# Kernel optimization log

Hardware: AMD Instinct MI355X
Metric: run time of the kernel (lower is better)

The kernel has to match this reference:

```python
import jax, jax.numpy as jnp
import numpy as np

H = 256; S = 64; AN = 16; D = 8; HH = 8; WW = 8; T = 32; N = 64; NV = 32
HG = 2 + 3 * H  # GRU hidden = sum(parser_sections) = 1 + 1 + 3*H


def _gru(x, w_ih, w_hh, b_ih, b_hh):
    """torch-style GRU over leading axis; x: [L, N, Hin] -> [L, N, HG]."""
    def step(h, xt):
        gi = xt @ w_ih.T + b_ih
        gh = h @ w_hh.T + b_hh
        ir, iz, inn = jnp.split(gi, 3, axis=-1)
        hr, hz, hn = jnp.split(gh, 3, axis=-1)
        r = jax.nn.sigmoid(ir + hr)
        z = jax.nn.sigmoid(iz + hz)
        n = jnp.tanh(inn + r * hn)
        h2 = (1 - z) * n + z * h
        return h2, h2
    h0 = jnp.zeros((x.shape[1], w_hh.shape[1]), x.dtype)
    _, ys = jax.lax.scan(step, h0, x)
    return ys


def _cos(e, m):  # e [N,H], m [N,S,H] -> [N,S]; matches F.cosine_similarity eps=1e-8
    num = jnp.einsum('nh,nsh->ns', e, m)
    den = jnp.linalg.norm(e, axis=-1)[:, None] * jnp.linalg.norm(m, axis=-1)
    return num / jnp.maximum(den, 1e-8)


def _l1norm(x):  # F.normalize(x, p=1, dim=-1)
    return x / jnp.maximum(jnp.abs(x).sum(-1, keepdims=True), 1e-12)


def setup_inputs():
    key = jax.random.key(0)
    ks = jax.random.split(key, 16)
    sc = lambda k, shape, fan: jax.random.normal(k, shape, jnp.float32) / np.float32(np.sqrt(fan))
    return dict(
        base=jax.random.normal(ks[0], (T, N, D, HH, WW), jnp.float32),
        interactable=(jax.random.uniform(ks[1], (T, N, AN - 5)) < 0.5).astype(jnp.float32),
        rnn_hxs=jnp.zeros((1, N, 1 + AN + 1 + H + S), jnp.float32),
        emb=sc(ks[2], (NV, H), 1.0),
        gru_w_ih=sc(ks[3], (3 * HG, H), H),
        gru_w_hh=sc(ks[4], (3 * HG, HG), HG),
        gru_b_ih=jnp.zeros((3 * HG,), jnp.float32),
        gru_b_hh=jnp.zeros((3 * HG,), jnp.float32),
        conv0_w=sc(ks[5], (H, D * H), D * H),
        conv0_b=jnp.zeros((H,), jnp.float32),
        convs_w=sc(ks[6], (2, H, H), H),
        convs_b=jnp.zeros((2, H), jnp.float32),
        lin_w=sc(ks[7], (H, H * HH * WW), H * HH * WW),
        lin_b=jnp.zeros((H,), jnp.float32),
        psi_w=sc(ks[8], (H, H * AN), H * AN),
        psi_b=jnp.zeros((H,), jnp.float32),
        actor_w=sc(ks[9], (AN, H), H),
        actor_b=jnp.zeros((AN,), jnp.float32),
        critic_w=sc(ks[10], (1, H), H),
        critic_b=jnp.zeros((1,), jnp.float32),
        subtasks=jax.random.randint(ks[11], (N, S), 0, NV),
        actions=jax.random.randint(ks[12], (T, N), 0, AN),
    )


def reference(base, interactable, rnn_hxs, emb, gru_w_ih, gru_w_hh, gru_b_ih, gru_b_hh,
              conv0_w, conv0_b, convs_w, convs_b, lin_w, lin_b, psi_w, psi_b,
              actor_w, actor_b, critic_w, critic_b, subtasks, actions):
    # --- parser: GRU over the subtask token sequence ---
    rnn_in = emb[subtasks].transpose(1, 0, 2)                                    # [S, N, H]
    X = _gru(rnn_in, gru_w_ih, gru_w_hh, gru_b_ih, gru_b_hh).transpose(1, 0, 2)  # [N, S, HG]
    c, p0 = X[..., 0], X[..., 1]                                                 # [N, S]
    M = X[..., 2:2 + H]
    Mm = X[..., 2 + H:2 + 2 * H]
    Mp = X[..., 2 + 2 * H:]
    hx = rnn_hxs[0]
    new_ep = jnp.all(rnn_hxs == 0, axis=-1)[0]                                   # [N]
    p_init = jnp.where(new_ep[:, None], p0, hx[:, 1 + AN + 1 + H:])

    def f_net(base_t, r):
        n = base_t.shape[0]
        # outer product [N,H,d,h,w] -> [N, H*d, h, w], then 1x1 convs
        x = (base_t[:, None] * r[:, :, None, None, None]).reshape(n, H * D, HH, WW)
        x = jax.nn.relu(jnp.einsum('nchw,oc->nohw', x, conv0_w) + conv0_b[None, :, None, None])
        for i in range(convs_w.shape[0]):
            x = jax.nn.relu(jnp.einsum('nchw,oc->nohw', x, convs_w[i]) + convs_b[i][None, :, None, None])
        return jax.nn.relu(x.reshape(n, -1) @ lin_w.T + lin_b)

    def step(p, xs):
        base_t, inter_t, a_t = xs
        ps = jax.nn.softmax(p, axis=-1)
        r = jnp.einsum('ns,nsh->nh', ps, M)                                      # memory read
        s = f_net(base_t, r)
        dprobs = jax.nn.softmax(s @ actor_w.T + actor_b, axis=-1)
        nonzero = jnp.pad(inter_t, ((0, 0), (5, 0)), constant_values=1.0)        # [N, AN]
        probs = dprobs * nonzero
        deficit = 1.0 - probs.sum(-1, keepdims=True)
        probs = probs + _l1norm(nonzero) * deficit
        probs = _l1norm(jnp.clip(probs, 0.0, 1.0))
        a_oh = jax.nn.one_hot(a_t, AN, dtype=s.dtype)
        e = (s[:, :, None] * a_oh[:, None, :]).reshape(s.shape[0], H * AN) @ psi_w.T + psi_b
        p_new = ps + c * _cos(e, Mp) - c * _cos(e, Mm)                           # memory write
        v = s @ critic_w.T + critic_b
        out = jnp.concatenate([a_t[:, None].astype(s.dtype), probs, v, s, p_new], axis=-1)
        return p_new, out

    _, hx_out = jax.lax.scan(step, p_init, (base, interactable, actions))        # [T, N, 338]
    return hx_out, hx_out[-1:]
```

## Files before the change

kernel.cpp:

```cpp
#include <hip/hip_runtime.h>
#include <math.h>

constexpr int cH  = 256;
constexpr int cS  = 64;
constexpr int cAN = 16;
constexpr int cD  = 8;
constexpr int cT  = 32;
constexpr int cN  = 64;
constexpr int cHG = 770;
constexpr int cG3 = 2310;
constexpr int cOW = 338;
constexpr int XLD = 800;
constexpr int GLD = 832;
constexpr int MLD = 2496;
constexpr int PROW = 2560;

__global__ __launch_bounds__(256) void k_gitab(const float* __restrict__ emb,
                                               const float* __restrict__ w_ih,
                                               const float* __restrict__ b_ih,
                                               float* __restrict__ gitp) {
  int v = blockIdx.y;
  int j = blockIdx.x * 256 + threadIdx.x;
  __shared__ float es[cH];
  es[threadIdx.x] = emb[v * cH + threadIdx.x];
  __syncthreads();
  if (j < cG3) {
    float acc = b_ih[j];
    const float* wr = w_ih + (size_t)j * cH;
    #pragma unroll 8
    for (int h = 0; h < cH; ++h) acc += wr[h] * es[h];
    int g = j / cHG, kk = j - g * cHG;
    gitp[(size_t)v * MLD + g * GLD + kk] = acc;
  }
}

__global__ __launch_bounds__(256) void k_wpad(const float* __restrict__ whh,
                                              float* __restrict__ wpadG) {
  int idx = blockIdx.x * 256 + threadIdx.x;
  if (idx < PROW * XLD) {
    int row = idx / XLD, col = idx - row * XLD;
    int g = row / GLD, k = row - g * GLD;
    wpadG[idx] = (g < 3 && k < cHG && col < cHG)
                     ? whh[(size_t)(g * cHG + k) * cHG + col] : 0.f;
  }
}

__global__ __launch_bounds__(256) void k_psiperm(const float* __restrict__ psi_w,
                                                 float* __restrict__ psip) {
  int idx = blockIdx.x * 256 + threadIdx.x;
  int a = idx >> 16, h = (idx >> 8) & 255, o = idx & 255;
  psip[idx] = psi_w[((size_t)o * cH + h) * cAN + a];
}

__global__ __launch_bounds__(256) void k_gru_gemm(const float* __restrict__ wpadG,
                                                  const float* __restrict__ X,
                                                  float* __restrict__ part, int s) {
  int tid = threadIdx.x;
  int tile = blockIdx.x % 40;
  int ks   = blockIdx.x / 40;
  int g = tile / 13, kt = tile - g * 13;
  int cbase = (ks <= 2) ? ks * 13 : 38;
  int ccnt  = (ks < 2) ? 13 : 12;
  int kbase = cbase * 16;
  int csz = ccnt * 16;

  __shared__ float Bst[208][68];
  __shared__ float As[2][16][68];

  const float* bsrc = wpadG + ((size_t)(g * GLD + kt * 64)) * XLD + kbase;
  for (int i = tid; i < 64 * 208; i += 256) {
    int jl = i / 208, k2l = i - jl * 208;
    if (k2l < csz) Bst[k2l][jl] = bsrc[(size_t)jl * XLD + k2l];
  }

  int tm = tid & 15, tj = tid >> 4;
  int lrow = tid >> 2, lcol = (tid & 3) * 4;
  __syncthreads();

  float acc[4][4] = {};
  const float* Xp = X + ((size_t)lrow * cS + (s - 1)) * XLD + kbase;
  float4 av = *(const float4*)(Xp + lcol);
  for (int c = 0; c < ccnt; ++c) {
    int buf = c & 1;
    As[buf][lcol + 0][lrow] = av.x;
    As[buf][lcol + 1][lrow] = av.y;
    As[buf][lcol + 2][lrow] = av.z;
    As[buf][lcol + 3][lrow] = av.w;
    __syncthreads();
    if (c + 1 < ccnt) av = *(const float4*)(Xp + (c + 1) * 16 + lcol);
    #pragma unroll
    for (int kk = 0; kk < 16; ++kk) {
      float4 a4 = *(const float4*)&As[buf][kk][tm * 4];
      float4 b4 = *(const float4*)&Bst[c * 16 + kk][tj * 4];
      acc[0][0] += a4.x * b4.x; acc[0][1] += a4.x * b4.y; acc[0][2] += a4.x * b4.z; acc[0][3] += a4.x * b4.w;
      acc[1][0] += a4.y * b4.x; acc[1][1] += a4.y * b4.y; acc[1][2] += a4.y * b4.z; acc[1][3] += a4.y * b4.w;
      acc[2][0] += a4.z * b4.x; acc[2][1] += a4.z * b4.y; acc[2][2] += a4.z * b4.z; acc[2][3] += a4.z * b4.w;
      acc[3][0] += a4.w * b4.x; acc[3][1] += a4.w * b4.y; acc[3][2] += a4.w * b4.z; acc[3][3] += a4.w * b4.w;
    }
    __syncthreads();
  }
  float* pw = part + (size_t)ks * (64 * PROW) + (size_t)(g * GLD + kt * 64);
  #pragma unroll
  for (int i = 0; i < 4; ++i) {
    *(float4*)(pw + (size_t)(tm * 4 + i) * PROW + tj * 4) =
        make_float4(acc[i][0], acc[i][1], acc[i][2], acc[i][3]);
  }
}

__global__ __launch_bounds__(256) void k_gru_gate(const float* __restrict__ part,
                                                  const float* __restrict__ bhh,
                                                  const float* __restrict__ gitp,
                                                  const int* __restrict__ subtasks,
                                                  float* __restrict__ X, int s) {
  int kq = blockIdx.x, m = blockIdx.y, tid = threadIdx.x;
  if (tid >= 200) return;
  int k = kq * 200 + tid;
  float* xrow = X + ((size_t)m * cS + s) * XLD;
  if (k >= cHG) { if (k < XLD) xrow[k] = 0.f; return; }
  float accr = 0.f, accz = 0.f, accn = 0.f;
  if (s > 0) {
    const float* pm = part + (size_t)m * PROW;
    #pragma unroll
    for (int q = 0; q < 4; ++q) {
      const float* pq = pm + (size_t)q * (64 * PROW);
      accr += pq[k];
      accz += pq[GLD + k];
      accn += pq[2 * GLD + k];
    }
  }
  int v = subtasks[m * cS + s];
  const float* git = gitp + (size_t)v * MLD;
  float rg = 1.f / (1.f + expf(-(git[k]           + accr + bhh[k])));
  float zg = 1.f / (1.f + expf(-(git[GLD + k]     + accz + bhh[cHG + k])));
  float ng = tanhf(git[2 * GLD + k] + rg * (accn + bhh[2 * cHG + k]));
  float hp = (s > 0) ? X[((size_t)m * cS + (s - 1)) * XLD + k] : 0.f;
  xrow[k] = (1.f - zg) * ng + zg * hp;
}

__global__ __launch_bounds__(256) void k_pinit(const float* __restrict__ hxs,
                                               const float* __restrict__ X,
                                               float* __restrict__ psb,
                                               float* __restrict__ r,
                                               float* __restrict__ nMp,
                                               float* __restrict__ nMm) {
  int n = blockIdx.x, tid = threadIdx.x;
  __shared__ int anynz;
  __shared__ float pss[cS];
  __shared__ float mx, sm;
  if (tid == 0) anynz = 0;
  __syncthreads();
  int nz = (hxs[n * cOW + tid] != 0.f) ? 1 : 0;
  if (tid + 256 < cOW) nz |= (hxs[n * cOW + tid + 256] != 0.f) ? 1 : 0;
  if (nz) anynz = 1;
  __syncthreads();
  bool newep = (anynz == 0);
  if (tid < cS) {
    const float* xr = X + ((size_t)n * cS + tid) * XLD;
    float p0 = xr[1];
    float pv = newep ? p0 : hxs[n * cOW + 1 + cAN + 1 + cH + tid];
    pss[tid] = pv;
    float sp = 0.f, smn = 0.f;
    for (int h = 0; h < cH; ++h) {
      float vp = xr[2 + 2 * cH + h]; sp += vp * vp;
      float vm = xr[2 + cH + h];     smn += vm * vm;
    }
    nMp[n * cS + tid] = sqrtf(sp);
    nMm[n * cS + tid] = sqrtf(smn);
  }
  __syncthreads();
  if (tid == 0) { float m = pss[0]; for (int i = 1; i < cS; ++i) m = fmaxf(m, pss[i]); mx = m; }
  __syncthreads();
  if (tid < cS) pss[tid] = expf(pss[tid] - mx);
  __syncthreads();
  if (tid == 0) { float s = 0.f; for (int i = 0; i < cS; ++i) s += pss[i]; sm = s; }
  __syncthreads();
  if (tid < cS) { pss[tid] /= sm; psb[n * cS + tid] = pss[tid]; }
  __syncthreads();
  float acc = 0.f;
  for (int s2 = 0; s2 < cS; ++s2)
    acc += pss[s2] * X[((size_t)n * cS + s2) * XLD + 2 + tid];
  r[n * cH + tid] = acc;
}

__global__ __launch_bounds__(256) void k_front(const float* __restrict__ r,
                                               const float* __restrict__ base,
                                               const float* __restrict__ cw,
                                               const float* __restrict__ cb,
                                               float* __restrict__ x1T, int t) {
  int o = blockIdx.x, tid = threadIdx.x;
  __shared__ float rsQ[64][65][4];
  __shared__ float w0s[64][9];

  #pragma unroll
  for (int it = 0; it < 16; ++it) {
    int flat4 = it * 256 + tid;
    int n = flat4 >> 6, hq = flat4 & 63;
    float4 v = *(const float4*)(r + n * cH + hq * 4);
    *(float4*)&rsQ[hq][n][0] = v;
  }
  __syncthreads();

  {
    int dg = tid >> 6, n = tid & 63;
    int d0 = dg * 2;
    const float* cwo = cw + (size_t)o * (cD * cH);
    float acc0 = 0.f, acc1 = 0.f;
    #pragma unroll 4
    for (int hq = 0; hq < 64; ++hq) {
      float4 rv = *(const float4*)&rsQ[hq][n][0];
      #pragma unroll
      for (int j = 0; j < 4; ++j) {
        float2 w = *(const float2*)(cwo + (hq * 4 + j) * 8 + d0);
        float rvj = ((const float*)&rv)[j];
        acc0 += w.x * rvj;
        acc1 += w.y * rvj;
      }
    }
    w0s[n][d0]     = acc0;
    w0s[n][d0 + 1] = acc1;
  }
  __syncthreads();

  {
    int q = tid >> 6, n = tid & 63;
    float w0[8];
    #pragma unroll
    for (int d = 0; d < 8; ++d) w0[d] = w0s[n][d];
    float bias = cb[o];
    const float4* b4 = (const float4*)(base + ((size_t)(t * cN + n) * cD) * 64);
    float* dst = x1T + (size_t)o * 4096 + n * 64 + q * 16;
    #pragma unroll
    for (int k = 0; k < 4; ++k) {
      float4 acc = make_float4(bias, bias, bias, bias);
      #pragma unroll
      for (int d = 0; d < 8; ++d) {
        float4 bv = b4[d * 16 + q * 4 + k];
        acc.x += w0[d] * bv.x; acc.y += w0[d] * bv.y;
        acc.z += w0[d] * bv.z; acc.w += w0[d] * bv.w;
      }
      acc.x = fmaxf(acc.x, 0.f); acc.y = fmaxf(acc.y, 0.f);
      acc.z = fmaxf(acc.z, 0.f); acc.w = fmaxf(acc.w, 0.f);
      *(float4*)(dst + k * 4) = acc;
    }
  }
}

__global__ __launch_bounds__(256) void k_gemmT(const float* __restrict__ AT,
                                               const float* __restrict__ W,
                                               const float* __restrict__ bias,
                                               float* __restrict__ C, int mode) {
  int nb = blockIdx.x, mb = blockIdx.y, tid = threadIdx.x;
  int tm = tid & 15, tj = tid >> 4;
  __shared__ float As[16][68];
  __shared__ float Bs[16][68];
  float acc[4][4] = {{0.f}};
  int lrow = tid >> 2, lcol = (tid & 3) * 4;
  int kr = tid >> 4, mc4 = (tid & 15) * 4;
  for (int kc = 0; kc < cH; kc += 16) {
    float4 av = *(const float4*)(AT + (size_t)(kc + kr) * 4096 + mb * 64 + mc4);
    float4 wv = *(const float4*)(W + (size_t)(nb * 64 + lrow) * cH + kc + lcol);
    *(float4*)&As[kr][mc4] = av;
    Bs[lcol][lrow] = wv.x; Bs[lcol + 1][lrow] = wv.y; Bs[lcol + 2][lrow] = wv.z; Bs[lcol + 3][lrow] = wv.w;
    __syncthreads();
    #pragma unroll
    for (int kk = 0; kk < 16; ++kk) {
      float4 a4 = *(const float4*)&As[kk][tm * 4];
      float4 b4 = *(const float4*)&Bs[kk][tj * 4];
      acc[0][0] += a4.x * b4.x; acc[0][1] += a4.x * b4.y; acc[0][2] += a4.x * b4.z; acc[0][3] += a4.x * b4.w;
      acc[1][0] += a4.y * b4.x; acc[1][1] += a4.y * b4.y; acc[1][2] += a4.y * b4.z; acc[1][3] += a4.y * b4.w;
      acc[2][0] += a4.z * b4.x; acc[2][1] += a4.z * b4.y; acc[2][2] += a4.z * b4.z; acc[2][3] += a4.z * b4.w;
      acc[3][0] += a4.w * b4.x; acc[3][1] += a4.w * b4.y; acc[3][2] += a4.w * b4.z; acc[3][3] += a4.w * b4.w;
    }
    __syncthreads();
  }
  if (mode == 0) {
    #pragma unroll
    for (int j = 0; j < 4; ++j) {
      int o = nb * 64 + tj * 4 + j;
      float bv = bias[o];
      float4 o4;
      o4.x = fmaxf(acc[0][j] + bv, 0.f);
      o4.y = fmaxf(acc[1][j] + bv, 0.f);
      o4.z = fmaxf(acc[2][j] + bv, 0.f);
      o4.w = fmaxf(acc[3][j] + bv, 0.f);
      *(float4*)(C + (size_t)o * 4096 + mb * 64 + tm * 4) = o4;
    }
  } else {
    #pragma unroll
    for (int j = 0; j < 4; ++j) {
      int o = nb * 64 + tj * 4 + j;
      float bv = bias[o];
      float4 o4;
      o4.x = fmaxf(acc[0][j] + bv, 0.f);
      o4.y = fmaxf(acc[1][j] + bv, 0.f);
      o4.z = fmaxf(acc[2][j] + bv, 0.f);
      o4.w = fmaxf(acc[3][j] + bv, 0.f);
      *(float4*)(C + (size_t)mb * (64 * cH) + (size_t)o * 64 + tm * 4) = o4;
    }
  }
}

__global__ __launch_bounds__(256) void k_lin(const float* __restrict__ A,
                                             const float* __restrict__ W,
                                             float* __restrict__ part) {
  int nb = blockIdx.x, kcb = blockIdx.y, tid = threadIdx.x;
  int tm = tid & 15, tj = tid >> 4;
  __shared__ float As[16][68];
  __shared__ float Bs[16][68];
  float acc[4][4] = {{0.f}};
  int lrow = tid >> 2, lcol = (tid & 3) * 4;
  for (int kc = 0; kc < 256; kc += 16) {
    float4 av = *(const float4*)(A + (size_t)lrow * 16384 + kcb * 256 + kc + lcol);
    float4 wv = *(const float4*)(W + (size_t)(nb * 64 + lrow) * 16384 + kcb * 256 + kc + lcol);
    As[lcol][lrow] = av.x; As[lcol + 1][lrow] = av.y; As[lcol + 2][lrow] = av.z; As[lcol + 3][lrow] = av.w;
    Bs[lcol][lrow] = wv.x; Bs[lcol + 1][lrow] = wv.y; Bs[lcol + 2][lrow] = wv.z; Bs[lcol + 3][lrow] = wv.w;
    __syncthreads();
    #pragma unroll
    for (int kk = 0; kk < 16; ++kk) {
      float4 a4 = *(const float4*)&As[kk][tm * 4];
      float4 b4 = *(const float4*)&Bs[kk][tj * 4];
      acc[0][0] += a4.x * b4.x; acc[0][1] += a4.x * b4.y; acc[0][2] += a4.x * b4.z; acc[0][3] += a4.x * b4.w;
      acc[1][0] += a4.y * b4.x; acc[1][1] += a4.y * b4.y; acc[1][2] += a4.y * b4.z; acc[1][3] += a4.y * b4.w;
      acc[2][0] += a4.z * b4.x; acc[2][1] += a4.z * b4.y; acc[2][2] += a4.z * b4.z; acc[2][3] += a4.z * b4.w;
      acc[3][0] += a4.w * b4.x; acc[3][1] += a4.w * b4.y; acc[3][2] += a4.w * b4.z; acc[3][3] += a4.w * b4.w;
    }
    __syncthreads();
  }
  #pragma unroll
  for (int i = 0; i < 4; ++i) {
    int n = tm * 4 + i;
    float4 o4 = make_float4(acc[i][0], acc[i][1], acc[i][2], acc[i][3]);
    *(float4*)(part + ((size_t)kcb * cN + n) * cH + nb * 64 + tj * 4) = o4;
  }
}

__global__ __launch_bounds__(256) void k_tail(const float* __restrict__ part,
                                              const float* __restrict__ lin_b,
                                              const float* __restrict__ actor_w,
                                              const float* __restrict__ actor_b,
                                              const float* __restrict__ critic_w,
                                              const float* __restrict__ critic_b,
                                              const float* __restrict__ psip,
                                              const float* __restrict__ psi_b,
                                              const float* __restrict__ inter,
                                              const int* __restrict__ actions,
                                              const float* __restrict__ X,
                                              const float* __restrict__ nMp,
                                              const float* __restrict__ nMm,
                                              float* __restrict__ psb,
                                              float* __restrict__ r,
                                              float* __restrict__ out, int t) {
  int n = blockIdx.x, tid = threadIdx.x;
  __shared__ float ss[cH];
  __shared__ float es[cH];
  __shared__ float lg[cAN], dp[cAN], nzv[cAN], prb[cAN];
  __shared__ float red[256];
  __shared__ float ared[16][17];
  __shared__ float cred[2][4][64];
  __shared__ float enorm_s;
  __shared__ float pns[cS];
  __shared__ float mx2, sm2;
  float* orow = out + ((size_t)t * cN + n) * cOW;
  float acc = lin_b[tid];
  for (int kc = 0; kc < 64; ++kc) acc += part[((size_t)kc * cN + n) * cH + tid];
  float sv = fmaxf(acc, 0.f);
  ss[tid] = sv;
  orow[1 + cAN + 1 + tid] = sv;
  __syncthreads();
  {
    int a = tid & 15, hg = tid >> 4;
    float pa = 0.f;
    const float* wr = actor_w + a * cH + hg * 16;
    const float* sh = &ss[hg * 16];
    #pragma unroll
    for (int hh2 = 0; hh2 < 16; ++hh2) pa += wr[hh2] * sh[hh2];
    ared[a][hg] = pa;
  }
  __syncthreads();
  if (tid < cAN) {
    float a = actor_b[tid];
    #pragma unroll
    for (int i = 0; i < 16; ++i) a += ared[tid][i];
    lg[tid] = a;
  }
  __syncthreads();
  if (tid < cAN) {
    float m = lg[0];
    for (int i = 1; i < cAN; ++i) m = fmaxf(m, lg[i]);
    dp[tid] = expf(lg[tid] - m);
  }
  __syncthreads();
  if (tid < cAN) {
    float s = 0.f;
    for (int i = 0; i < cAN; ++i) s += dp[i];
    float dprob = dp[tid] / s;
    float nv = (tid < 5) ? 1.f : inter[((size_t)t * cN + n) * (cAN - 5) + (tid - 5)];
    nzv[tid] = nv;
    prb[tid] = dprob * nv;
  }
  __syncthreads();
  if (tid < cAN) {
    float sp = 0.f, sn = 0.f;
    for (int i = 0; i < cAN; ++i) { sp += prb[i]; sn += nzv[i]; }
    float deficit = 1.f - sp;
    float v2 = prb[tid] + (nzv[tid] / fmaxf(sn, 1e-12f)) * deficit;
    prb[tid] = fminf(fmaxf(v2, 0.f), 1.f);
  }
  __syncthreads();
  if (tid < cAN) {
    float s = 0.f;
    for (int i = 0; i < cAN; ++i) s += prb[i];
    orow[1 + tid] = prb[tid] / fmaxf(s, 1e-12f);
  }
  int at = actions[t * cN + n];
  {
    float a = psi_b[tid];
    for (int h = 0; h < cH; ++h) a += psip[((size_t)at * cH + h) * cH + tid] * ss[h];
    es[tid] = a;
    red[tid] = a * a;
  }
  __syncthreads();
  for (int st = 128; st > 0; st >>= 1) {
    if (tid < st) red[tid] += red[tid + st];
    __syncthreads();
  }
  if (tid == 0) enorm_s = sqrtf(red[0]);
  __syncthreads();
  float enorm = enorm_s;
  red[tid] = critic_w[tid] * ss[tid];
  __syncthreads();
  for (int st = 128; st > 0; st >>= 1) {
    if (tid < st) red[tid] += red[tid + st];
    __syncthreads();
  }
  if (tid == 0) {
    orow[1 + cAN] = red[0] + critic_b[0];
    orow[0] = (float)at;
  }
  {
    int s2 = tid & 63, hg = tid >> 6;
    const float* xr = X + ((size_t)n * cS + s2) * XLD;
    const float* xp = xr + 2 + 2 * cH + hg * 64;
    const float* xm = xr + 2 + cH + hg * 64;
    const float* ep = &es[hg * 64];
    float dpp = 0.f, dmm = 0.f;
    #pragma unroll 8
    for (int h2 = 0; h2 < 64; ++h2) {
      float ev = ep[h2];
      dpp += ev * xp[h2];
      dmm += ev * xm[h2];
    }
    cred[0][hg][s2] = dpp;
    cred[1][hg][s2] = dmm;
  }
  __syncthreads();
  if (tid < cS) {
    float dpp = cred[0][0][tid] + cred[0][1][tid] + cred[0][2][tid] + cred[0][3][tid];
    float dmm = cred[1][0][tid] + cred[1][1][tid] + cred[1][2][tid] + cred[1][3][tid];
    const float* xr = X + ((size_t)n * cS + tid) * XLD;
    float cP = dpp / fmaxf(enorm * nMp[n * cS + tid], 1e-8f);
    float cM = dmm / fmaxf(enorm * nMm[n * cS + tid], 1e-8f);
    float cc = xr[0];
    float pn = psb[n * cS + tid] + cc * cP - cc * cM;
    pns[tid] = pn;
    orow[1 + cAN + 1 + cH + tid] = pn;
  }
  __threadfence_block();
  __syncthreads();
  if (t == cT - 1) {
    float* orow2 = out + (size_t)cT * cN * cOW + (size_t)n * cOW;
    orow2[tid] = orow[tid];
    if (tid + 256 < cOW) orow2[tid + 256] = orow[tid + 256];
  }
  if (tid == 0) { float m2 = pns[0]; for (int i = 1; i < cS; ++i) m2 = fmaxf(m2, pns[i]); mx2 = m2; }
  __syncthreads();
  if (tid < cS) pns[tid] = expf(pns[tid] - mx2);
  __syncthreads();
  if (tid == 0) { float s2 = 0.f; for (int i = 0; i < cS; ++i) s2 += pns[i]; sm2 = s2; }
  __syncthreads();
  if (tid < cS) { pns[tid] /= sm2; psb[n * cS + tid] = pns[tid]; }
  __syncthreads();
  float acc2 = 0.f;
  for (int s2 = 0; s2 < cS; ++s2)
    acc2 += pns[s2] * X[((size_t)n * cS + s2) * XLD + 2 + tid];
  r[n * cH + tid] = acc2;
}

extern "C" void kernel_launch(void* const* d_in, const int* in_sizes, int n_in,
                              void* d_out, int out_size, void* d_ws, size_t ws_size,
                              hipStream_t stream) {
  const float* base     = (const float*)d_in[0];
  const float* inter    = (const float*)d_in[1];
  const float* hxs      = (const float*)d_in[2];
  const float* emb      = (const float*)d_in[3];
  const float* w_ih     = (const float*)d_in[4];
  const float* w_hh     = (const float*)d_in[5];
  const float* b_ih     = (const float*)d_in[6];
  const float* b_hh     = (const float*)d_in[7];
  const float* conv0_w  = (const float*)d_in[8];
  const float* conv0_b  = (const float*)d_in[9];
  const float* convs_w  = (const float*)d_in[10];
  const float* convs_b  = (const float*)d_in[11];
  const float* lin_w    = (const float*)d_in[12];
  const float* lin_b    = (const float*)d_in[13];
  const float* psi_w    = (const float*)d_in[14];
  const float* psi_b    = (const float*)d_in[15];
  const float* actor_w  = (const float*)d_in[16];
  const float* actor_b  = (const float*)d_in[17];
  const float* critic_w = (const float*)d_in[18];
  const float* critic_b = (const float*)d_in[19];
  const int*   subtasks = (const int*)d_in[20];
  const int*   actions  = (const int*)d_in[21];
  float* out = (float*)d_out;
  float* ws  = (float*)d_ws;

  float* gitp  = ws + 0;
  float* psb   = ws + 0;
  float* r     = ws + 4096;
  float* nMp   = ws + 20480;
  float* nMm   = ws + 24576;
  float* X     = ws + 79872;
  float* wpadG = ws + 3356672;
  float* psip  = ws + 3356672;
  float* x1T   = ws + 4405248;
  float* part  = x1T;
  float* partG = ws + 5404672;
  float* x2T   = ws + 5453824;
  float* x3t   = ws + 6502400;

  k_gitab<<<dim3(10, 32), 256, 0, stream>>>(emb, w_ih, b_ih, gitp);
  k_wpad<<<8000, 256, 0, stream>>>(w_hh, wpadG);
  k_gru_gate<<<dim3(4, 64), 256, 0, stream>>>(partG, b_hh, gitp, subtasks, X, 0);
  for (int s = 1; s < cS; ++s) {
    k_gru_gemm<<<160, 256, 0, stream>>>(wpadG, X, partG, s);
    k_gru_gate<<<dim3(4, 64), 256, 0, stream>>>(partG, b_hh, gitp, subtasks, X, s);
  }
  k_psiperm<<<4096, 256, 0, stream>>>(psi_w, psip);
  k_pinit<<<64, 256, 0, stream>>>(hxs, X, psb, r, nMp, nMm);
  for (int t = 0; t < cT; ++t) {
    k_front<<<256, 256, 0, stream>>>(r, base, conv0_w, conv0_b, x1T, t);
    k_gemmT<<<dim3(4, 64), 256, 0, stream>>>(x1T, convs_w, convs_b, x2T, 0);
    k_gemmT<<<dim3(4, 64), 256, 0, stream>>>(x2T, convs_w + 65536, convs_b + 256, x3t, 1);
    k_lin<<<dim3(4, 64), 256, 0, stream>>>(x3t, lin_w, part);
    k_tail<<<64, 256, 0, stream>>>(part, lin_b, actor_w, actor_b, critic_w, critic_b,
                                   psip, psi_b, inter, actions, X, nMp, nMm,
                                   psb, r, out, t);
  }
}
```

Before: 4.611 ms.

## Fuse conv0 into first conv GEMM and move r-to-weight projection into tail

Result: slower. 5.887 ms (+27.7%).

```diff
diff --git a/kernel.cpp b/kernel.cpp
--- a/kernel.cpp
+++ b/kernel.cpp
@@ -139,13 +139,16 @@
 
 __global__ __launch_bounds__(256) void k_pinit(const float* __restrict__ hxs,
                                                const float* __restrict__ X,
+                                               const float* __restrict__ cw,
                                                float* __restrict__ psb,
                                                float* __restrict__ r,
                                                float* __restrict__ nMp,
-                                               float* __restrict__ nMm) {
+                                               float* __restrict__ nMm,
+                                               float* __restrict__ w0r) {
   int n = blockIdx.x, tid = threadIdx.x;
   __shared__ int anynz;
   __shared__ float pss[cS];
+  __shared__ float rsf[cH];
   __shared__ float mx, sm;
   if (tid == 0) anynz = 0;
   __syncthreads();
@@ -180,76 +183,102 @@
   for (int s2 = 0; s2 < cS; ++s2)
     acc += pss[s2] * X[((size_t)n * cS + s2) * XLD + 2 + tid];
   r[n * cH + tid] = acc;
-}
-
-__global__ __launch_bounds__(256) void k_front(const float* __restrict__ r,
-                                               const float* __restrict__ base,
-                                               const float* __restrict__ cw,
-                                               const float* __restrict__ cb,
-                                               float* __restrict__ x1T, int t) {
-  int o = blockIdx.x, tid = threadIdx.x;
-  __shared__ float rsQ[64][65][4];
-  __shared__ float w0s[64][9];
-
+  rsf[tid] = acc;
+  __syncthreads();
+  {
+    const float* cwo = cw + (size_t)tid * (cD * cH);
+    float a0=0,a1=0,a2=0,a3=0,a4=0,a5=0,a6=0,a7=0;
+    #pragma unroll 4
+    for (int h = 0; h < cH; ++h) {
+      float rv = rsf[h];
+      float4 wa = *(const float4*)(cwo + h * 8);
+      float4 wb = *(const float4*)(cwo + h * 8 + 4);
+      a0 += wa.x * rv; a1 += wa.y * rv; a2 += wa.z * rv; a3 += wa.w * rv;
+      a4 += wb.x * rv; a5 += wb.y * rv; a6 += wb.z * rv; a7 += wb.w * rv;
+    }
+    float* wd = w0r + (size_t)n * 2048 + tid * 8;
+    *(float4*)(wd)     = make_float4(a0, a1, a2, a3);
+    *(float4*)(wd + 4) = make_float4(a4, a5, a6, a7);
+  }
+}
+
+__global__ __launch_bounds__(256) void k_conv1f(const float* __restrict__ w0r,
+                                                const float* __restrict__ base,
+                                                const float* __restrict__ cb0,
+                                                const float* __restrict__ W1,
+                                                const float* __restrict__ b1,
+                                                float* __restrict__ y1T, int t) {
+  int b = blockIdx.x, tid = threadIdx.x;
+  int n  = (b & 7) | ((b >> 5) << 3);
+  int nb = (b >> 3) & 3;
+  __shared__ float x1s[256][68];
+  __shared__ float w0s[256][9];
+  __shared__ float bs[8][64];
+  __shared__ float Bs[16][68];
+  {
+    const float* src = w0r + (size_t)n * 2048 + tid * 8;
+    float4 va = *(const float4*)(src);
+    float4 vb = *(const float4*)(src + 4);
+    *(float4*)&w0s[tid][0] = va;
+    *(float4*)&w0s[tid][4] = vb;
+    w0s[tid][8] = cb0[tid];
+  }
+  if (tid < 128) {
+    int d = tid >> 4, c4 = (tid & 15) * 4;
+    *(float4*)&bs[d][c4] =
+        *(const float4*)(base + ((size_t)(t * cN + n) * cD + d) * 64 + c4);
+  }
+  __syncthreads();
+  {
+    int wv = tid >> 6, ln = tid & 63;
+    for (int oi = 0; oi < 64; ++oi) {
+      int o = wv * 64 + oi;
+      float acc = w0s[o][8];
+      #pragma unroll
+      for (int d = 0; d < 8; ++d) acc += w0s[o][d] * bs[d][ln];
+      x1s[o][ln] = fmaxf(acc, 0.f);
+    }
+  }
+  __syncthreads();
+  int tm = tid & 15, tj = tid >> 4;
+  int lrow = tid >> 2, lcol = (tid & 3) * 4;
+  float acc[4][4] = {{0.f}};
+  for (int kc = 0; kc < cH; kc += 16) {
+    float4 wv4 = *(const float4*)(W1 + (size_t)(nb * 64 + lrow) * cH + kc + lcol);
+    Bs[lcol][lrow] = wv4.x; Bs[lcol + 1][lrow] = wv4.y;
+    Bs[lcol + 2][lrow] = wv4.z; Bs[lcol + 3][lrow] = wv4.w;
+    __syncthreads();
+    #pragma unroll
+    for (int kk = 0; kk < 16; ++kk) {
+      float4 a4 = *(const float4*)&x1s[kc + kk][tm * 4];
+      float4 b4 = *(const float4*)&Bs[kk][tj * 4];
+      acc[0][0] += a4.x * b4.x; acc[0][1] += a4.x * b4.y; acc[0][2] += a4.x * b4.z; acc[0][3] += a4.x * b4.w;
+      acc[1][0] += a4.y * b4.x; acc[1][1] += a4.y * b4.y; acc[1][2] += a4.y * b4.z; acc[1][3] += a4.y * b4.w;
+      acc[2][0] += a4.z * b4.x; acc[2][1] += a4.z * b4.y; acc[2][2] += a4.z * b4.z; acc[2][3] += a4.z * b4.w;
+      acc[3][0] += a4.w * b4.x; acc[3][1] += a4.w * b4.y; acc[3][2] += a4.w * b4.z; acc[3][3] += a4.w * b4.w;
+    }
+    __syncthreads();
+  }
   #pragma unroll
-  for (int it = 0; it < 16; ++it) {
-    int flat4 = it * 256 + tid;
-    int n = flat4 >> 6, hq = flat4 & 63;
-    float4 v = *(const float4*)(r + n * cH + hq * 4);
-    *(float4*)&rsQ[hq][n][0] = v;
-  }
-  __syncthreads();
-
-  {
-    int dg = tid >> 6, n = tid & 63;
-    int d0 = dg * 2;
-    const float* cwo = cw + (size_t)o * (cD * cH);
-    float acc0 = 0.f, acc1 = 0.f;
-    #pragma unroll 4
-    for (int hq = 0; hq < 64; ++hq) {
-      float4 rv = *(const float4*)&rsQ[hq][n][0];
-      #pragma unroll
-      for (int j = 0; j < 4; ++j) {
-        float2 w = *(const float2*)(cwo + (hq * 4 + j) * 8 + d0);
-        float rvj = ((const float*)&rv)[j];
-        acc0 += w.x * rvj;
-        acc1 += w.y * rvj;
-      }
-    }
-    w0s[n][d0]     = acc0;
-    w0s[n][d0 + 1] = acc1;
-  }
-  __syncthreads();
-
-  {
-    int q = tid >> 6, n = tid & 63;
-    float w0[8];
-    #pragma unroll
-    for (int d = 0; d < 8; ++d) w0[d] = w0s[n][d];
-    float bias = cb[o];
-    const float4* b4 = (const float4*)(base + ((size_t)(t * cN + n) * cD) * 64);
-    float* dst = x1T + (size_t)o * 4096 + n * 64 + q * 16;
-    #pragma unroll
-    for (int k = 0; k < 4; ++k) {
-      float4 acc = make_float4(bias, bias, bias, bias);
-      #pragma unroll
-      for (int d = 0; d < 8; ++d) {
-        float4 bv = b4[d * 16 + q * 4 + k];
-        acc.x += w0[d] * bv.x; acc.y += w0[d] * bv.y;
-        acc.z += w0[d] * bv.z; acc.w += w0[d] * bv.w;
-      }
-      acc.x = fmaxf(acc.x, 0.f); acc.y = fmaxf(acc.y, 0.f);
-      acc.z = fmaxf(acc.z, 0.f); acc.w = fmaxf(acc.w, 0.f);
-      *(float4*)(dst + k * 4) = acc;
-    }
-  }
-}
-
-__global__ __launch_bounds__(256) void k_gemmT(const float* __restrict__ AT,
+  for (int j = 0; j < 4; ++j) {
+    int o = nb * 64 + tj * 4 + j;
+    float bv = b1[o];
+    float4 o4;
+    o4.x = fmaxf(acc[0][j] + bv, 0.f);
+    o4.y = fmaxf(acc[1][j] + bv, 0.f);
+    o4.z = fmaxf(acc[2][j] + bv, 0.f);
+    o4.w = fmaxf(acc[3][j] + bv, 0.f);
+    *(float4*)(y1T + (size_t)o * 4096 + n * 64 + tm * 4) = o4;
+  }
+}
+
+__global__ __launch_bounds__(256) void k_conv2(const float* __restrict__ AT,
                                                const float* __restrict__ W,
                                                const float* __restrict__ bias,
-                                               float* __restrict__ C, int mode) {
-  int nb = blockIdx.x, mb = blockIdx.y, tid = threadIdx.x;
+                                               float* __restrict__ C) {
+  int b = blockIdx.x, tid = threadIdx.x;
+  int n  = (b & 7) | ((b >> 5) << 3);
+  int nb = (b >> 3) & 3;
   int tm = tid & 15, tj = tid >> 4;
   __shared__ float As[16][68];
   __shared__ float Bs[16][68];
@@ -257,7 +286,7 @@
   int lrow = tid >> 2, lcol = (tid & 3) * 4;
   int kr = tid >> 4, mc4 = (tid & 15) * 4;
   for (int kc = 0; kc < cH; kc += 16) {
-    float4 av = *(const float4*)(AT + (size_t)(kc + kr) * 4096 + mb * 64 + mc4);
+    float4 av = *(const float4*)(AT + (size_t)(kc + kr) * 4096 + n * 64 + mc4);
     float4 wv = *(const float4*)(W + (size_t)(nb * 64 + lrow) * cH + kc + lcol);
     *(float4*)&As[kr][mc4] = av;
     Bs[lcol][lrow] = wv.x; Bs[lcol + 1][lrow] = wv.y; Bs[lcol + 2][lrow] = wv.z; Bs[lcol + 3][lrow] = wv.w;
@@ -273,37 +302,25 @@
     }
     __syncthreads();
   }
-  if (mode == 0) {
-    #pragma unroll
-    for (int j = 0; j < 4; ++j) {
-      int o = nb * 64 + tj * 4 + j;
-      float bv = bias[o];
-      float4 o4;
-      o4.x = fmaxf(acc[0][j] + bv, 0.f);
-      o4.y = fmaxf(acc[1][j] + bv, 0.f);
-      o4.z = fmaxf(acc[2][j] + bv, 0.f);
-      o4.w = fmaxf(acc[3][j] + bv, 0.f);
-      *(float4*)(C + (size_t)o * 4096 + mb * 64 + tm * 4) = o4;
-    }
-  } else {
-    #pragma unroll
-    for (int j = 0; j < 4; ++j) {
-      int o = nb * 64 + tj * 4 + j;
-      float bv = bias[o];
-      float4 o4;
-      o4.x = fmaxf(acc[0][j] + bv, 0.f);
-      o4.y = fmaxf(acc[1][j] + bv, 0.f);
-      o4.z = fmaxf(acc[2][j] + bv, 0.f);
-      o4.w = fmaxf(acc[3][j] + bv, 0.f);
-      *(float4*)(C + (size_t)mb * (64 * cH) + (size_t)o * 64 + tm * 4) = o4;
-    }
+  #pragma unroll
+  for (int j = 0; j < 4; ++j) {
+    int o = nb * 64 + tj * 4 + j;
+    float bv = bias[o];
+    float4 o4;
+    o4.x = fmaxf(acc[0][j] + bv, 0.f);
+    o4.y = fmaxf(acc[1][j] + bv, 0.f);
+    o4.z = fmaxf(acc[2][j] + bv, 0.f);
+    o4.w = fmaxf(acc[3][j] + bv, 0.f);
+    *(float4*)(C + (size_t)n * (64 * cH) + (size_t)o * 64 + tm * 4) = o4;
   }
 }
 
 __global__ __launch_bounds__(256) void k_lin(const float* __restrict__ A,
                                              const float* __restrict__ W,
                                              float* __restrict__ part) {
-  int nb = blockIdx.x, kcb = blockIdx.y, tid = threadIdx.x;
+  int b = blockIdx.x, tid = threadIdx.x;
+  int kcb = (b & 7) | ((b >> 5) << 3);
+  int nb  = (b >> 3) & 3;
   int tm = tid & 15, tj = tid >> 4;
   __shared__ float As[16][68];
   __shared__ float Bs[16][68];
@@ -347,12 +364,15 @@
                                               const float* __restrict__ X,
                                               const float* __restrict__ nMp,
                                               const float* __restrict__ nMm,
+                                              const float* __restrict__ cw,
                                               float* __restrict__ psb,
                                               float* __restrict__ r,
+                                              float* __restrict__ w0r,
                                               float* __restrict__ out, int t) {
   int n = blockIdx.x, tid = threadIdx.x;
   __shared__ float ss[cH];
   __shared__ float es[cH];
+  __shared__ float rsf[cH];
   __shared__ float lg[cAN], dp[cAN], nzv[cAN], prb[cAN];
   __shared__ float red[256];
   __shared__ float ared[16][17];
@@ -484,6 +504,23 @@
   for (int s2 = 0; s2 < cS; ++s2)
     acc2 += pns[s2] * X[((size_t)n * cS + s2) * XLD + 2 + tid];
   r[n * cH + tid] = acc2;
+  rsf[tid] = acc2;
+  __syncthreads();
+  if (t < cT - 1) {
+    const float* cwo = cw + (size_t)tid * (cD * cH);
+    float a0=0,a1=0,a2=0,a3=0,a4=0,a5=0,a6=0,a7=0;
+    #pragma unroll 4
+    for (int h = 0; h < cH; ++h) {
+      float rv = rsf[h];
+      float4 wa = *(const float4*)(cwo + h * 8);
+      float4 wb = *(const float4*)(cwo + h * 8 + 4);
+      a0 += wa.x * rv; a1 += wa.y * rv; a2 += wa.z * rv; a3 += wa.w * rv;
+      a4 += wb.x * rv; a5 += wb.y * rv; a6 += wb.z * rv; a7 += wb.w * rv;
+    }
+    float* wd = w0r + (size_t)n * 2048 + tid * 8;
+    *(float4*)(wd)     = make_float4(a0, a1, a2, a3);
+    *(float4*)(wd + 4) = make_float4(a4, a5, a6, a7);
+  }
 }
 
 extern "C" void kernel_launch(void* const* d_in, const int* in_sizes, int n_in,
@@ -514,19 +551,19 @@
   float* out = (float*)d_out;
   float* ws  = (float*)d_ws;
 
-  float* gitp  = ws + 0;
-  float* psb   = ws + 0;
-  float* r     = ws + 4096;
-  float* nMp   = ws + 20480;
-  float* nMm   = ws + 24576;
-  float* X     = ws + 79872;
-  float* wpadG = ws + 3356672;
-  float* psip  = ws + 3356672;
-  float* x1T   = ws + 4405248;
-  float* part  = x1T;
-  float* partG = ws + 5404672;
-  float* x2T   = ws + 5453824;
-  float* x3t   = ws + 6502400;
+  float* gitp    = ws + 0;
+  float* psb     = ws + 0;
+  float* r       = ws + 4096;
+  float* nMp     = ws + 20480;
+  float* nMm     = ws + 24576;
+  float* X       = ws + 79872;
+  float* wpadG   = ws + 3356672;
+  float* psip    = ws + 3356672;
+  float* y1T     = ws + 4405248;
+  float* partG   = ws + 5404672;
+  float* x3t     = ws + 5453824;
+  float* linpart = ws + 6502400;
+  float* w0r     = ws + 7550976;
 
   k_gitab<<<dim3(10, 32), 256, 0, stream>>>(emb, w_ih, b_ih, gitp);
   k_wpad<<<8000, 256, 0, stream>>>(w_hh, wpadG);
@@ -536,14 +573,13 @@
     k_gru_gate<<<dim3(4, 64), 256, 0, stream>>>(partG, b_hh, gitp, subtasks, X, s);
   }
   k_psiperm<<<4096, 256, 0, stream>>>(psi_w, psip);
-  k_pinit<<<64, 256, 0, stream>>>(hxs, X, psb, r, nMp, nMm);
+  k_pinit<<<64, 256, 0, stream>>>(hxs, X, conv0_w, psb, r, nMp, nMm, w0r);
   for (int t = 0; t < cT; ++t) {
-    k_front<<<256, 256, 0, stream>>>(r, base, conv0_w, conv0_b, x1T, t);
-    k_gemmT<<<dim3(4, 64), 256, 0, stream>>>(x1T, convs_w, convs_b, x2T, 0);
-    k_gemmT<<<dim3(4, 64), 256, 0, stream>>>(x2T, convs_w + 65536, convs_b + 256, x3t, 1);
-    k_lin<<<dim3(4, 64), 256, 0, stream>>>(x3t, lin_w, part);
-    k_tail<<<64, 256, 0, stream>>>(part, lin_b, actor_w, actor_b, critic_w, critic_b,
-                                   psip, psi_b, inter, actions, X, nMp, nMm,
-                                   psb, r, out, t);
-  }
-}
+    k_conv1f<<<256, 256, 0, stream>>>(w0r, base, conv0_b, convs_w, convs_b, y1T, t);
+    k_conv2<<<256, 256, 0, stream>>>(y1T, convs_w + 65536, convs_b + 256, x3t);
+    k_lin<<<256, 256, 0, stream>>>(x3t, lin_w, linpart);
+    k_tail<<<64, 256, 0, stream>>>(linpart, lin_b, actor_w, actor_b, critic_w, critic_b,
+                                   psip, psi_b, inter, actions, X, nMp, nMm, conv0_w,
+                                   psb, r, w0r, out, t);
+  }
+}
```

## Fuse GRU gate into next-step GEMM with double-buffered partial sums

Applied to the files above, without the earlier changes.

Result: slower. 8.449 ms (+83.2%).

```diff
diff --git a/kernel.cpp b/kernel.cpp
--- a/kernel.cpp
+++ b/kernel.cpp
@@ -52,20 +52,27 @@
   psip[idx] = psi_w[((size_t)o * cH + h) * cAN + a];
 }
 
-__global__ __launch_bounds__(256) void k_gru_gemm(const float* __restrict__ wpadG,
-                                                  const float* __restrict__ X,
-                                                  float* __restrict__ part, int s) {
+__global__ __launch_bounds__(256) void k_gru_fused(const float* __restrict__ wpadG,
+                                                   const float* __restrict__ bhh,
+                                                   const float* __restrict__ gitp,
+                                                   const int* __restrict__ subtasks,
+                                                   float* __restrict__ X,
+                                                   float* __restrict__ pOut,
+                                                   const float* __restrict__ pIn,
+                                                   int s) {
   int tid = threadIdx.x;
-  int tile = blockIdx.x % 40;
-  int ks   = blockIdx.x / 40;
+  int b = blockIdx.x;
+  int ks   = (b & 7) >> 1;
+  int tile = (b >> 3) * 2 + (b & 1);
   int g = tile / 13, kt = tile - g * 13;
   int cbase = (ks <= 2) ? ks * 13 : 38;
   int ccnt  = (ks < 2) ? 13 : 12;
   int kbase = cbase * 16;
   int csz = ccnt * 16;
+  bool writer = ((b >> 3) == 0) && ((b & 1) == 0);
 
   __shared__ float Bst[208][68];
-  __shared__ float As[2][16][68];
+  __shared__ float Xl[208][68];
 
   const float* bsrc = wpadG + ((size_t)(g * GLD + kt * 64)) * XLD + kbase;
   for (int i = tid; i < 64 * 208; i += 256) {
@@ -73,33 +80,66 @@
     if (k2l < csz) Bst[k2l][jl] = bsrc[(size_t)jl * XLD + k2l];
   }
 
+  if (s >= 2) {
+    for (int mi = 0; mi < 16; ++mi) {
+      int m = (tid >> 6) + 4 * mi;
+      int v = subtasks[m * cS + (s - 1)];
+      const float* git = gitp + (size_t)v * MLD;
+      const float* pm  = pIn + (size_t)m * PROW;
+      const float* xprev = X + ((size_t)m * cS + (s - 2)) * XLD;
+      float* xw = X + ((size_t)m * cS + (s - 1)) * XLD;
+      #pragma unroll
+      for (int kc = 0; kc < 4; ++kc) {
+        int k2l = (tid & 63) + kc * 64;
+        if (k2l < csz) {
+          int k = kbase + k2l;
+          float val = 0.f;
+          if (k < cHG) {
+            float accr = 0.f, accz = 0.f, accn = 0.f;
+            #pragma unroll
+            for (int q = 0; q < 4; ++q) {
+              const float* pq = pm + (size_t)q * (64 * PROW);
+              accr += pq[k];
+              accz += pq[GLD + k];
+              accn += pq[2 * GLD + k];
+            }
+            float rg = 1.f / (1.f + expf(-(git[k]           + accr + bhh[k])));
+            float zg = 1.f / (1.f + expf(-(git[GLD + k]     + accz + bhh[cHG + k])));
+            float ng = tanhf(git[2 * GLD + k] + rg * (accn + bhh[2 * cHG + k]));
+            val = (1.f - zg) * ng + zg * xprev[k];
+          }
+          Xl[k2l][m] = val;
+          if (writer) xw[k] = val;
+        }
+      }
+    }
+  } else {
+    for (int mi = 0; mi < 16; ++mi) {
+      int m = (tid >> 6) + 4 * mi;
+      const float* xr = X + ((size_t)m * cS) * XLD + kbase;
+      #pragma unroll
+      for (int kc = 0; kc < 4; ++kc) {
+        int k2l = (tid & 63) + kc * 64;
+        if (k2l < csz) Xl[k2l][m] = xr[k2l];
+      }
+    }
+  }
+  __syncthreads();
+
   int tm = tid & 15, tj = tid >> 4;
-  int lrow = tid >> 2, lcol = (tid & 3) * 4;
-  __syncthreads();
-
   float acc[4][4] = {};
-  const float* Xp = X + ((size_t)lrow * cS + (s - 1)) * XLD + kbase;
-  float4 av = *(const float4*)(Xp + lcol);
   for (int c = 0; c < ccnt; ++c) {
-    int buf = c & 1;
-    As[buf][lcol + 0][lrow] = av.x;
-    As[buf][lcol + 1][lrow] = av.y;
-    As[buf][lcol + 2][lrow] = av.z;
-    As[buf][lcol + 3][lrow] = av.w;
-    __syncthreads();
-    if (c + 1 < ccnt) av = *(const float4*)(Xp + (c + 1) * 16 + lcol);
     #pragma unroll
     for (int kk = 0; kk < 16; ++kk) {
-      float4 a4 = *(const float4*)&As[buf][kk][tm * 4];
+      float4 a4 = *(const float4*)&Xl[c * 16 + kk][tm * 4];
       float4 b4 = *(const float4*)&Bst[c * 16 + kk][tj * 4];
       acc[0][0] += a4.x * b4.x; acc[0][1] += a4.x * b4.y; acc[0][2] += a4.x * b4.z; acc[0][3] += a4.x * b4.w;
       acc[1][0] += a4.y * b4.x; acc[1][1] += a4.y * b4.y; acc[1][2] += a4.y * b4.z; acc[1][3] += a4.y * b4.w;
       acc[2][0] += a4.z * b4.x; acc[2][1] += a4.z * b4.y; acc[2][2] += a4.z * b4.z; acc[2][3] += a4.z * b4.w;
       acc[3][0] += a4.w * b4.x; acc[3][1] += a4.w * b4.y; acc[3][2] += a4.w * b4.z; acc[3][3] += a4.w * b4.w;
     }
-    __syncthreads();
-  }
-  float* pw = part + (size_t)ks * (64 * PROW) + (size_t)(g * GLD + kt * 64);
+  }
+  float* pw = pOut + (size_t)ks * (64 * PROW) + (size_t)(g * GLD + kt * 64);
   #pragma unroll
   for (int i = 0; i < 4; ++i) {
     *(float4*)(pw + (size_t)(tm * 4 + i) * PROW + tj * 4) =
@@ -514,27 +554,31 @@
   float* out = (float*)d_out;
   float* ws  = (float*)d_ws;
 
-  float* gitp  = ws + 0;
-  float* psb   = ws + 0;
-  float* r     = ws + 4096;
-  float* nMp   = ws + 20480;
-  float* nMm   = ws + 24576;
-  float* X     = ws + 79872;
-  float* wpadG = ws + 3356672;
-  float* psip  = ws + 3356672;
-  float* x1T   = ws + 4405248;
-  float* part  = x1T;
-  float* partG = ws + 5404672;
-  float* x2T   = ws + 5453824;
-  float* x3t   = ws + 6502400;
+  float* gitp   = ws + 0;
+  float* psb    = ws + 0;
+  float* r      = ws + 4096;
+  float* nMp    = ws + 20480;
+  float* nMm    = ws + 24576;
+  float* X      = ws + 79872;
+  float* wpadG  = ws + 3356672;
+  float* psip   = ws + 3356672;
+  float* x1T    = ws + 4405248;
+  float* part   = x1T;
+  float* partG  = ws + 5404672;
+  float* x2T    = ws + 5453824;
+  float* x3t    = ws + 6502400;
+  float* partG2 = ws + 6502400;
+
+  float* pbuf[2] = {partG, partG2};
 
   k_gitab<<<dim3(10, 32), 256, 0, stream>>>(emb, w_ih, b_ih, gitp);
   k_wpad<<<8000, 256, 0, stream>>>(w_hh, wpadG);
   k_gru_gate<<<dim3(4, 64), 256, 0, stream>>>(partG, b_hh, gitp, subtasks, X, 0);
-  for (int s = 1; s < cS; ++s) {
-    k_gru_gemm<<<160, 256, 0, stream>>>(wpadG, X, partG, s);
-    k_gru_gate<<<dim3(4, 64), 256, 0, stream>>>(partG, b_hh, gitp, subtasks, X, s);
-  }
+  for (int s = 1; s < cS; ++s)
+    k_gru_fused<<<160, 256, 0, stream>>>(wpadG, b_hh, gitp, subtasks, X,
+                                         pbuf[s & 1], pbuf[(s - 1) & 1], s);
+  k_gru_gate<<<dim3(4, 64), 256, 0, stream>>>(pbuf[(cS - 1) & 1], b_hh, gitp,
+                                              subtasks, X, cS - 1);
   k_psiperm<<<4096, 256, 0, stream>>>(psi_w, psip);
   k_pinit<<<64, 256, 0, stream>>>(hxs, X, psb, r, nMp, nMm);
   for (int t = 0; t < cT; ++t) {
```
